# Optimization experiments

Hardware: AMD Instinct MI355X
Metric: run time of the kernel (lower is better)

The kernel has to match this reference:

```python
import jax, jax.numpy as jnp
import numpy as np

B, S, D, H = 2, 2048, 2048, 16
HD = D // H


def setup_inputs() -> dict:
    key = jax.random.key(0)
    ks = jax.random.split(key, 9)
    scale = 0.02
    return {
        "x": jax.random.normal(ks[0], (B, S, D), dtype=jnp.float32),
        "wq_w": jax.random.normal(ks[1], (D, D), dtype=jnp.float32) * scale,
        "wq_b": jnp.zeros((D,), dtype=jnp.float32),
        "wk_w": jax.random.normal(ks[2], (D, D), dtype=jnp.float32) * scale,
        "wk_b": jnp.zeros((D,), dtype=jnp.float32),
        "wv_w": jax.random.normal(ks[3], (D, D), dtype=jnp.float32) * scale,
        "wv_b": jnp.zeros((D,), dtype=jnp.float32),
        "wo_w": jax.random.normal(ks[4], (D, D), dtype=jnp.float32) * scale,
        "wo_b": jnp.zeros((D,), dtype=jnp.float32),
    }


def reference(x, wq_w, wq_b, wk_w, wk_b, wv_w, wv_b, wo_w, wo_b):
    # torch Linear: y = x @ W.T + b
    q = x @ wq_w.T + wq_b  # [B,S,D]
    k = x @ wk_w.T + wk_b
    v = x @ wv_w.T + wv_b
    # [B,S,D] -> [B,H,S,HD]
    q = q.reshape(B, S, H, HD).transpose(0, 2, 1, 3)
    k = k.reshape(B, S, H, HD).transpose(0, 2, 1, 3)
    v = v.reshape(B, S, H, HD).transpose(0, 2, 1, 3)
    # scores [B,H,S,S], scaled by sqrt(d_dim) as in the original (not head_dim)
    scores = jnp.einsum("bhid,bhjd->bhij", q, k) / np.float32(np.sqrt(D))
    # faithful reproduction of the module's triu/transpose masking:
    m = jnp.swapaxes(jnp.triu(scores), -2, -1)  # lower-tri, zeros elsewhere
    p = jax.nn.softmax(m, axis=-2)              # softmax over dim=-2, zeros included
    a = jnp.swapaxes(jnp.triu(p), -2, -1)       # [B,H,S,S]
    attn = jnp.einsum("bhij,bhjd->bhid", a, v)  # [B,H,S,HD]
    concat = attn.transpose(0, 2, 1, 3).reshape(B, S, D)
    return concat @ wo_w.T + wo_b
```

## Files before the change

kernel.cpp:

```cpp
#include <hip/hip_runtime.h>

#define BB 2
#define SS 2048
#define DD 2048
#define HH 16
#define HDIM 128
#define MTOK (BB*SS)
#define BHH (BB*HH)
#define NCHUNK 16
#define QKN (2*DD)

typedef __attribute__((ext_vector_type(8))) __bf16 bf16x8;
typedef __attribute__((ext_vector_type(4))) float f32x4;
typedef __attribute__((ext_vector_type(8))) int i32x8;
typedef __attribute__((ext_vector_type(4))) int i32x4;

__device__ __forceinline__ unsigned short f2bf(float f) {
  unsigned u = __float_as_uint(f);
  u += 0x7FFFu + ((u >> 16) & 1u);
  return (unsigned short)(u >> 16);
}
__device__ __forceinline__ float bf2f(unsigned short s) {
  return __uint_as_float(((unsigned)s) << 16);
}
__device__ __forceinline__ unsigned char f2e4m3(float f) {
  int pk = __builtin_amdgcn_cvt_pk_fp8_f32(f, f, 0, false);
  return (unsigned char)(pk & 0xFF);
}

#define GLOAD_LDS16(src, dst)                                                   \
  __builtin_amdgcn_global_load_lds(                                             \
      (const void __attribute__((address_space(1)))*)(src),                     \
      (void __attribute__((address_space(3)))*)(dst), 16, 0, 0)

__device__ __forceinline__ void barrier_raw() {
  asm volatile("" ::: "memory");
  __builtin_amdgcn_s_barrier();
  asm volatile("" ::: "memory");
}

__global__ void cvt_x_dual(const float* __restrict__ in,
                           unsigned short* __restrict__ outb,
                           unsigned int* __restrict__ out8, int n4) {
  int i = blockIdx.x * blockDim.x + threadIdx.x;
  if (i < n4) {
    float4 v = ((const float4*)in)[i];
    ushort4 o;
    o.x = f2bf(v.x); o.y = f2bf(v.y); o.z = f2bf(v.z); o.w = f2bf(v.w);
    ((ushort4*)outb)[i] = o;
    int p0 = __builtin_amdgcn_cvt_pk_fp8_f32(v.x, v.y, 0, false);
    int p1 = __builtin_amdgcn_cvt_pk_fp8_f32(v.z, v.w, 0, false);
    out8[i] = (unsigned)(p0 & 0xFFFF) | ((unsigned)(p1 & 0xFFFF) << 16);
  }
}

__global__ void cvt_w_all(const float* __restrict__ wq, const float* __restrict__ wk,
                          const float* __restrict__ wv, const float* __restrict__ wo,
                          const float* __restrict__ wqb, const float* __restrict__ wkb,
                          unsigned int* __restrict__ out8,
                          unsigned short* __restrict__ outb,
                          float* __restrict__ biasqk) {
  int blk = blockIdx.x;
  int tid = threadIdx.x;
  if (blk < 8192) {
    int i = blk * 256 + tid;
    int sel = i >> 20, r = i & 0xFFFFF;
    const float* src = sel == 0 ? wq : wk;
    float4 v = ((const float4*)src)[r];
    int p0 = __builtin_amdgcn_cvt_pk_fp8_f32(v.x, v.y, 0, false);
    int p1 = __builtin_amdgcn_cvt_pk_fp8_f32(v.z, v.w, 0, false);
    out8[i] = (unsigned)(p0 & 0xFFFF) | ((unsigned)(p1 & 0xFFFF) << 16);
  } else if (blk < 16384) {
    int i = (blk - 8192) * 256 + tid;
    int sel = i >> 20, r = i & 0xFFFFF;
    const float* src = sel == 0 ? wv : wo;
    float4 v = ((const float4*)src)[r];
    ushort4 o;
    o.x = f2bf(v.x); o.y = f2bf(v.y); o.z = f2bf(v.z); o.w = f2bf(v.w);
    ((ushort4*)outb)[i] = o;
  } else {
    int i = (blk - 16384) * 256 + tid;
    biasqk[i] = (i < DD) ? wqb[i] : wkb[i - DD];
  }
}

template <bool OUT_BF16>
__global__ __launch_bounds__(256, 2) void gemm_bt8(
    const __bf16* __restrict__ A, const __bf16* __restrict__ W,
    const float* __restrict__ bias, void* __restrict__ Cout,
    int M, int N, int K) {
  __shared__ unsigned char lds[2][32768];
  const int t = threadIdx.x;
  const int lane = t & 63, wave = t >> 6;
  const int quad = lane >> 4, l16 = lane & 15;
  const int m0 = blockIdx.y * 128;
  const int n0 = blockIdx.x * 128;
  const int wm = (wave & 1) * 64, wn = (wave >> 1) * 64;

  const __bf16* sA[4];
  const __bf16* sB[4];
#pragma unroll
  for (int c = 0; c < 4; ++c) {
    int L = c * 256 + t;
    int row = L >> 3, p = L & 7;
    int sc = (p ^ (row & 7)) * 8;
    sA[c] = A + (size_t)(m0 + row) * K + sc;
    sB[c] = W + (size_t)(n0 + row) * K + sc;
  }
  const int phk0 = (quad ^ (l16 & 7)) * 16;
  const int phk1 = ((4 + quad) ^ (l16 & 7)) * 16;

  f32x4 acc[4][4] = {};

  const int NT = K >> 6;

#pragma unroll
  for (int c = 0; c < 4; ++c)
    GLOAD_LDS16(sA[c], &lds[0][(c * 256 + wave * 64) * 16]);
#pragma unroll
  for (int c = 0; c < 4; ++c)
    GLOAD_LDS16(sB[c], &lds[0][16384 + (c * 256 + wave * 64) * 16]);

  for (int tt = 0; tt < NT; ++tt) {
    const int cur = tt & 1;
    const bool pf = (tt + 1 < NT);
    const int k1 = (tt + 1) << 6;

    if (pf) {
#pragma unroll
      for (int c = 0; c < 4; ++c)
        GLOAD_LDS16(sA[c] + k1, &lds[cur ^ 1][(c * 256 + wave * 64) * 16]);
      asm volatile("s_waitcnt vmcnt(4)" ::: "memory");
    } else {
      asm volatile("s_waitcnt vmcnt(0)" ::: "memory");
    }
    barrier_raw();
    {
      bf16x8 af[4], bfv[4];
#pragma unroll
      for (int mt = 0; mt < 4; ++mt)
        af[mt] = *(const bf16x8*)&lds[cur][(wm + mt * 16 + l16) * 128 + phk0];
#pragma unroll
      for (int nt = 0; nt < 4; ++nt)
        bfv[nt] =
            *(const bf16x8*)&lds[cur][16384 + (wn + nt * 16 + l16) * 128 + phk0];
      __builtin_amdgcn_s_setprio(1);
#pragma unroll
      for (int mt = 0; mt < 4; ++mt)
#pragma unroll
        for (int nt = 0; nt < 4; ++nt)
          acc[mt][nt] = __builtin_amdgcn_mfma_f32_16x16x32_bf16(
              af[mt], bfv[nt], acc[mt][nt], 0, 0, 0);
      __builtin_amdgcn_s_setprio(0);
    }

    if (pf) {
#pragma unroll
      for (int c = 0; c < 4; ++c)
        GLOAD_LDS16(sB[c] + k1, &lds[cur ^ 1][16384 + (c * 256 + wave * 64) * 16]);
    }
    barrier_raw();
    {
      bf16x8 af[4], bfv[4];
#pragma unroll
      for (int mt = 0; mt < 4; ++mt)
        af[mt] = *(const bf16x8*)&lds[cur][(wm + mt * 16 + l16) * 128 + phk1];
#pragma unroll
      for (int nt = 0; nt < 4; ++nt)
        bfv[nt] =
            *(const bf16x8*)&lds[cur][16384 + (wn + nt * 16 + l16) * 128 + phk1];
      __builtin_amdgcn_s_setprio(1);
#pragma unroll
      for (int mt = 0; mt < 4; ++mt)
#pragma unroll
        for (int nt = 0; nt < 4; ++nt)
          acc[mt][nt] = __builtin_amdgcn_mfma_f32_16x16x32_bf16(
              af[mt], bfv[nt], acc[mt][nt], 0, 0, 0);
      __builtin_amdgcn_s_setprio(0);
    }
    barrier_raw();
  }

#pragma unroll
  for (int mt = 0; mt < 4; ++mt) {
#pragma unroll
    for (int nt = 0; nt < 4; ++nt) {
      int col = n0 + wn + nt * 16 + l16;
      float bv = bias[col];
#pragma unroll
      for (int r = 0; r < 4; ++r) {
        int row = m0 + wm + mt * 16 + quad * 4 + r;
        float v = acc[mt][nt][r] + bv;
        if constexpr (OUT_BF16)
          ((unsigned short*)Cout)[(size_t)row * N + col] = f2bf(v);
        else
          ((float*)Cout)[(size_t)row * N + col] = v;
      }
    }
  }
}

__global__ __launch_bounds__(256, 2) void gemm_qk8(
    const unsigned char* __restrict__ A8, const unsigned char* __restrict__ W8,
    const float* __restrict__ bias, unsigned char* __restrict__ Cout,
    int M, int N, int K) {
  __shared__ unsigned char lds[2][32768];
  const int t = threadIdx.x;
  const int lane = t & 63, wave = t >> 6;
  const int quad = lane >> 4, l16 = lane & 15;
  const int m0 = blockIdx.y * 128;
  const int n0 = blockIdx.x * 128;
  const int wm = (wave & 1) * 64, wn = (wave >> 1) * 64;

  const unsigned char* sA[4];
  const unsigned char* sB[4];
#pragma unroll
  for (int c = 0; c < 4; ++c) {
    int L = c * 256 + t;
    int row = L >> 3, p = L & 7;
    int sc = (p ^ (row & 7)) * 16;
    sA[c] = A8 + (size_t)(m0 + row) * K + sc;
    sB[c] = W8 + (size_t)(n0 + row) * K + sc;
  }
  const int p0 = (2 * quad) ^ (l16 & 7);

  f32x4 acc[4][4] = {};

  const int NT = K >> 7;

#pragma unroll
  for (int c = 0; c < 4; ++c)
    GLOAD_LDS16(sA[c], &lds[0][(c * 256 + wave * 64) * 16]);
#pragma unroll
  for (int c = 0; c < 4; ++c)
    GLOAD_LDS16(sB[c], &lds[0][16384 + (c * 256 + wave * 64) * 16]);

  for (int tt = 0; tt < NT; ++tt) {
    const int cur = tt & 1;
    const bool pf = (tt + 1 < NT);
    const int k1 = (tt + 1) << 7;

    if (pf) {
#pragma unroll
      for (int c = 0; c < 4; ++c)
        GLOAD_LDS16(sA[c] + k1, &lds[cur ^ 1][(c * 256 + wave * 64) * 16]);
      asm volatile("s_waitcnt vmcnt(4)" ::: "memory");
    } else {
      asm volatile("s_waitcnt vmcnt(0)" ::: "memory");
    }
    barrier_raw();
    i32x8 af[4];
    {
#pragma unroll
      for (int mt = 0; mt < 4; ++mt) {
        int ra = (wm + mt * 16 + l16) * 128 + p0 * 16;
        ((i32x4*)&af[mt])[0] = *(const i32x4*)&lds[cur][ra];
        ((i32x4*)&af[mt])[1] = *(const i32x4*)&lds[cur][ra ^ 16];
      }
      i32x8 bv[2];
#pragma unroll
      for (int nt = 0; nt < 2; ++nt) {
        int rb = 16384 + (wn + nt * 16 + l16) * 128 + p0 * 16;
        ((i32x4*)&bv[nt])[0] = *(const i32x4*)&lds[cur][rb];
        ((i32x4*)&bv[nt])[1] = *(const i32x4*)&lds[cur][rb ^ 16];
      }
      __builtin_amdgcn_s_setprio(1);
#pragma unroll
      for (int mt = 0; mt < 4; ++mt)
#pragma unroll
        for (int nt = 0; nt < 2; ++nt)
          acc[mt][nt] = __builtin_amdgcn_mfma_scale_f32_16x16x128_f8f6f4(
              af[mt], bv[nt], acc[mt][nt], 0, 0, 0, 127, 0, 127);
      __builtin_amdgcn_s_setprio(0);
    }

    if (pf) {
#pragma unroll
      for (int c = 0; c < 4; ++c)
        GLOAD_LDS16(sB[c] + k1, &lds[cur ^ 1][16384 + (c * 256 + wave * 64) * 16]);
    }
    barrier_raw();
    {
      i32x8 bv[2];
#pragma unroll
      for (int nt = 0; nt < 2; ++nt) {
        int rb = 16384 + (wn + (nt + 2) * 16 + l16) * 128 + p0 * 16;
        ((i32x4*)&bv[nt])[0] = *(const i32x4*)&lds[cur][rb];
        ((i32x4*)&bv[nt])[1] = *(const i32x4*)&lds[cur][rb ^ 16];
      }
      __builtin_amdgcn_s_setprio(1);
#pragma unroll
      for (int mt = 0; mt < 4; ++mt)
#pragma unroll
        for (int nt = 0; nt < 2; ++nt)
          acc[mt][nt + 2] = __builtin_amdgcn_mfma_scale_f32_16x16x128_f8f6f4(
              af[mt], bv[nt], acc[mt][nt + 2], 0, 0, 0, 127, 0, 127);
      __builtin_amdgcn_s_setprio(0);
    }
    barrier_raw();
  }

#pragma unroll
  for (int mt = 0; mt < 4; ++mt) {
#pragma unroll
    for (int nt = 0; nt < 4; ++nt) {
      int col = n0 + wn + nt * 16 + l16;
      float bv = bias[col];
#pragma unroll
      for (int r = 0; r < 4; ++r) {
        int row = m0 + wm + mt * 16 + quad * 4 + r;
        Cout[(size_t)row * N + col] = f2e4m3(acc[mt][nt][r] + bv);
      }
    }
  }
}

__global__ __launch_bounds__(256, 4) void qk_rowsum8(
    const unsigned char* __restrict__ q8, const unsigned char* __restrict__ k8,
    float* __restrict__ denomA, float* __restrict__ denomB,
    float* __restrict__ diag) {
  __shared__ unsigned char lK[2][128 * 128];
  __shared__ float redS[4][64];
  __shared__ float redD[4][64];
  const int t = threadIdx.x;
  const int lane = t & 63, wave = t >> 6;
  const int quad = lane >> 4, l16 = lane & 15;
  const int bh = blockIdx.y;
  const int b = bh >> 4, h = bh & 15;
  const int pair = blockIdx.x >> 1;
  const int half = blockIdx.x & 1;
  const float C = 0.03187935771f;
  const f32x4 fz = {0.f, 0.f, 0.f, 0.f};

  int soff[4];
#pragma unroll
  for (int c = 0; c < 4; ++c) {
    int L = c * 256 + t;
    int row = L >> 3, p = L & 7;
    soff[c] = row * QKN + ((p ^ (row & 7)) * 16);
  }
  const int p0 = (2 * quad) ^ (l16 & 7);
  int bo[2];
#pragma unroll
  for (int nt = 0; nt < 2; ++nt)
    bo[nt] = (wave * 32 + nt * 16 + l16) * 128 + p0 * 16;

  const unsigned char* kbase = k8 + (size_t)(b * SS) * QKN + h * HDIM;

  for (int sub = 0; sub < 2; ++sub) {
    const int tile = (sub == 0) ? pair : 31 - pair;
    const int i0 = tile * 64;
    const int jbase = i0 & ~127;
    const int ntile = (SS - jbase) >> 7;

    i32x8 af[4];
    {
      const unsigned char* qbase =
          q8 + (size_t)(b * SS + i0 + l16) * QKN + h * HDIM + quad * 32;
#pragma unroll
      for (int mt = 0; mt < 4; ++mt)
        af[mt] = *(const i32x8*)(qbase + (size_t)(mt * 16) * QKN);
    }

    float rowacc[4][4] = {};

    int kidx = half;
    if (kidx < ntile) {
      {
        const unsigned char* src = kbase + (size_t)(jbase + kidx * 128) * QKN;
#pragma unroll
        for (int c = 0; c < 4; ++c)
          GLOAD_LDS16(src + soff[c], &lK[0][(c * 256 + wave * 64) * 16]);
      }
      asm volatile("s_waitcnt vmcnt(0)" ::: "memory");
      __syncthreads();
      int cur = 0;
      for (; kidx < ntile; kidx += 2, cur ^= 1) {
        if (kidx + 2 < ntile) {
          const unsigned char* src =
              kbase + (size_t)(jbase + (kidx + 2) * 128) * QKN;
#pragma unroll
          for (int c = 0; c < 4; ++c)
            GLOAD_LDS16(src + soff[c], &lK[cur ^ 1][(c * 256 + wave * 64) * 16]);
        }
        const unsigned char* lkc = lK[cur];
        const int j0 = jbase + kidx * 128;
        if (kidx == 0) {
          float dloc[4][4] = {};
#pragma unroll
          for (int nt = 0; nt < 2; ++nt) {
            i32x8 bf;
            ((i32x4*)&bf)[0] = *(const i32x4*)(lkc + bo[nt]);
            ((i32x4*)&bf)[1] = *(const i32x4*)(lkc + (bo[nt] ^ 16));
            f32x4 acc[4];
#pragma unroll
            for (int mt = 0; mt < 4; ++mt)
              acc[mt] = __builtin_amdgcn_mfma_scale_f32_16x16x128_f8f6f4(
                  af[mt], bf, fz, 0, 0, 0, 127, 0, 127);
            const int colg = j0 + wave * 32 + nt * 16 + l16;
#pragma unroll
            for (int mt = 0; mt < 4; ++mt)
#pragma unroll
              for (int r = 0; r < 4; ++r) {
                int rg = i0 + mt * 16 + quad * 4 + r;
                float e = (colg >= rg)
                              ? __builtin_amdgcn_exp2f(acc[mt][r] * C) : 0.f;
                rowacc[mt][r] += e;
                if (colg == rg) dloc[mt][r] = e;
              }
          }
#pragma unroll
          for (int mt = 0; mt < 4; ++mt)
#pragma unroll
            for (int r = 0; r < 4; ++r) {
              float d = dloc[mt][r];
#pragma unroll
              for (int off = 1; off < 16; off <<= 1) d += __shfl_xor(d, off, 64);
              if (l16 == 0) redD[wave][mt * 16 + quad * 4 + r] = d;
            }
        } else {
#pragma unroll
          for (int nt = 0; nt < 2; ++nt) {
            i32x8 bf;
            ((i32x4*)&bf)[0] = *(const i32x4*)(lkc + bo[nt]);
            ((i32x4*)&bf)[1] = *(const i32x4*)(lkc + (bo[nt] ^ 16));
            f32x4 acc[4];
#pragma unroll
            for (int mt = 0; mt < 4; ++mt)
              acc[mt] = __builtin_amdgcn_mfma_scale_f32_16x16x128_f8f6f4(
                  af[mt], bf, fz, 0, 0, 0, 127, 0, 127);
#pragma unroll
            for (int mt = 0; mt < 4; ++mt)
#pragma unroll
              for (int r = 0; r < 4; ++r)
                rowacc[mt][r] += __builtin_amdgcn_exp2f(acc[mt][r] * C);
          }
        }
        asm volatile("s_waitcnt vmcnt(0)" ::: "memory");
        __syncthreads();
      }
    }

    __syncthreads();
#pragma unroll
    for (int mt = 0; mt < 4; ++mt)
#pragma unroll
      for (int r = 0; r < 4; ++r) {
        float s = rowacc[mt][r];
#pragma unroll
        for (int off = 1; off < 16; off <<= 1) s += __shfl_xor(s, off, 64);
        if (l16 == 0) redS[wave][mt * 16 + quad * 4 + r] = s;
      }
    __syncthreads();
    if (t < 64) {
      const int rg = i0 + t;
      float s = redS[0][t] + redS[1][t] + redS[2][t] + redS[3][t];
      if (half == 0) {
        denomA[bh * SS + rg] = (float)rg + s;
        diag[bh * SS + rg] = redD[0][t] + redD[1][t] + redD[2][t] + redD[3][t];
      } else {
        denomB[bh * SS + rg] = s;
      }
    }
  }
}

__global__ void scan_pass1(const __bf16* __restrict__ v0,
                           float* __restrict__ csum) {
  int blk = blockIdx.x;
  int bh = blk >> 4, c = blk & 15;
  int b = bh >> 4, h = bh & 15;
  int t = threadIdx.x;
  int rs = t >> 4, dg = t & 15;
  const unsigned short* base = (const unsigned short*)v0 +
      (size_t)(b * SS + c * 128 + rs * 8) * DD + h * HDIM + dg * 8;
  float s[8] = {0.f, 0.f, 0.f, 0.f, 0.f, 0.f, 0.f, 0.f};
#pragma unroll
  for (int i = 0; i < 8; ++i) {
    uint4 u = *(const uint4*)(base + (size_t)i * DD);
    const unsigned short* us = (const unsigned short*)&u;
#pragma unroll
    for (int j = 0; j < 8; ++j) s[j] += bf2f(us[j]);
  }
  __shared__ float red[16 * 128];
#pragma unroll
  for (int j = 0; j < 8; ++j) red[rs * 128 + dg * 8 + j] = s[j];
  __syncthreads();
  for (int st = 8; st >= 1; st >>= 1) {
    if (rs < st) {
#pragma unroll
      for (int j = 0; j < 8; ++j)
        red[rs * 128 + dg * 8 + j] += red[(rs + st) * 128 + dg * 8 + j];
    }
    __syncthreads();
  }
  if (rs == 0) {
#pragma unroll
    for (int j = 0; j < 8; ++j)
      csum[(size_t)blk * 128 + dg * 8 + j] = red[dg * 8 + j];
  }
}

__global__ void scan_pass2(const __bf16* __restrict__ v0,
                           const float* __restrict__ csum,
                           const float* __restrict__ denomA,
                           const float* __restrict__ denomB,
                           const float* __restrict__ diag,
                           unsigned short* __restrict__ ctx) {
  int blk = blockIdx.x;
  int bh = blk >> 4, c = blk & 15;
  int b = bh >> 4, h = bh & 15;
  int t = threadIdx.x;
  int rs = t >> 4, dg = t & 15;
  const unsigned short* vbase = (const unsigned short*)v0 +
      (size_t)(b * SS + c * 128 + rs * 8) * DD + h * HDIM + dg * 8;
  float vrow[8][8];
  float ls[8] = {0.f, 0.f, 0.f, 0.f, 0.f, 0.f, 0.f, 0.f};
#pragma unroll
  for (int i = 0; i < 8; ++i) {
    uint4 u = *(const uint4*)(vbase + (size_t)i * DD);
    const unsigned short* us = (const unsigned short*)&u;
#pragma unroll
    for (int j = 0; j < 8; ++j) {
      vrow[i][j] = bf2f(us[j]);
      ls[j] += vrow[i][j];
    }
  }
  __shared__ float red[16 * 128];
#pragma unroll
  for (int j = 0; j < 8; ++j) red[rs * 128 + dg * 8 + j] = ls[j];
  __syncthreads();

  float pre[8] = {0.f, 0.f, 0.f, 0.f, 0.f, 0.f, 0.f, 0.f};
  for (int cc = 0; cc < c; ++cc) {
    const float* cp = csum + (size_t)(bh * 16 + cc) * 128 + dg * 8;
#pragma unroll
    for (int j = 0; j < 8; ++j) pre[j] += cp[j];
  }
  for (int ss2 = 0; ss2 < rs; ++ss2) {
#pragma unroll
    for (int j = 0; j < 8; ++j) pre[j] += red[ss2 * 128 + dg * 8 + j];
  }

  int row0 = c * 128 + rs * 8;
  unsigned short* obase =
      ctx + (size_t)(b * SS + row0) * DD + h * HDIM + dg * 8;
  const float* dnA = denomA + bh * SS + row0;
  const float* dnB = denomB + bh * SS + row0;
  const float* dgp = diag + bh * SS + row0;
#pragma unroll
  for (int i = 0; i < 8; ++i) {
    float inv = 1.0f / (dnA[i] + dnB[i]);
    float dv = dgp[i];
    unsigned short o[8];
#pragma unroll
    for (int j = 0; j < 8; ++j) {
      float val = (pre[j] + dv * vrow[i][j]) * inv;
      o[j] = f2bf(val);
      pre[j] += vrow[i][j];
    }
    *(uint4*)(obase + (size_t)i * DD) = *(const uint4*)o;
  }
}

extern "C" void kernel_launch(void* const* d_in, const int* in_sizes, int n_in,
                              void* d_out, int out_size, void* d_ws, size_t ws_size,
                              hipStream_t stream) {
  (void)in_sizes; (void)n_in; (void)out_size; (void)ws_size;
  const float* x    = (const float*)d_in[0];
  const float* wq_w = (const float*)d_in[1];
  const float* wq_b = (const float*)d_in[2];
  const float* wk_w = (const float*)d_in[3];
  const float* wk_b = (const float*)d_in[4];
  const float* wv_w = (const float*)d_in[5];
  const float* wv_b = (const float*)d_in[6];
  const float* wo_w = (const float*)d_in[7];
  const float* wo_b = (const float*)d_in[8];

  char* ws = (char*)d_ws;
  size_t off = 0;
  auto alloc = [&](size_t bytes) {
    char* p = ws + off;
    off += (bytes + 255) & ~(size_t)255;
    return p;
  };
  unsigned short* xb   = (unsigned short*)alloc((size_t)MTOK * DD * 2);
  unsigned char*  x8   = (unsigned char*)alloc((size_t)MTOK * DD);
  unsigned char*  wqk8 = (unsigned char*)alloc((size_t)2 * DD * DD);
  unsigned short* wvo  = (unsigned short*)alloc((size_t)2 * DD * DD * 2);
  unsigned char*  qk8  = (unsigned char*)alloc((size_t)MTOK * QKN);
  unsigned short* v    = (unsigned short*)alloc((size_t)MTOK * DD * 2);
  unsigned short* ctx  = (unsigned short*)alloc((size_t)MTOK * DD * 2);
  float* biasqk = (float*)alloc((size_t)2 * DD * 4);
  float* denomA = (float*)alloc((size_t)BHH * SS * 4);
  float* denomB = (float*)alloc((size_t)BHH * SS * 4);
  float* diag   = (float*)alloc((size_t)BHH * SS * 4);
  float* csum   = (float*)alloc((size_t)BHH * NCHUNK * 128 * 4);

  {
    int n4 = MTOK * DD / 4;
    cvt_x_dual<<<n4 / 256, 256, 0, stream>>>(x, xb, (unsigned int*)x8, n4);
    cvt_w_all<<<16400, 256, 0, stream>>>(wq_w, wk_w, wv_w, wo_w, wq_b, wk_b,
                                         (unsigned int*)wqk8, wvo, biasqk);
  }

  gemm_qk8<<<dim3(QKN / 128, MTOK / 128), 256, 0, stream>>>(
      x8, wqk8, biasqk, qk8, MTOK, QKN, DD);

  gemm_bt8<true><<<dim3(DD / 128, MTOK / 128), 256, 0, stream>>>(
      (const __bf16*)xb, (const __bf16*)wvo, wv_b, v, MTOK, DD, DD);

  qk_rowsum8<<<dim3(32, BHH), 256, 0, stream>>>(
      qk8,
      qk8 + DD,
      denomA, denomB, diag);

  scan_pass1<<<BHH * NCHUNK, 256, 0, stream>>>((const __bf16*)v, csum);
  scan_pass2<<<BHH * NCHUNK, 256, 0, stream>>>((const __bf16*)v, csum,
                                               denomA, denomB, diag, ctx);

  gemm_bt8<false><<<dim3(DD / 128, MTOK / 128), 256, 0, stream>>>(
      (const __bf16*)ctx, (const __bf16*)(wvo + (size_t)DD * DD), wo_b,
      d_out, MTOK, DD, DD);
}
```

Measured before the change: 310.7 us.

## Load GEMM A operand directly to registers, stage only weights in LDS

Both the bf16 and fp8 GEMM kernels stop staging the A tile through shared memory. Each wave now reads its A fragments straight from global memory into registers, and only the weight tile is double-buffered in LDS. This halves LDS per block, which allows launch bounds of 4 blocks per CU, and it merges the two half-step barriers per K tile into one. The cost is that A rows are reread from global/L2 by each of the two wave columns instead of being shared. The A loads are also issued right before use with no prefetch, so their latency may be exposed.

Result: slower. 546.3 us (+75.9%).

```diff
diff --git a/kernel.cpp b/kernel.cpp
--- a/kernel.cpp
+++ b/kernel.cpp
@@ -85,11 +85,11 @@
 }
 
 template <bool OUT_BF16>
-__global__ __launch_bounds__(256, 2) void gemm_bt8(
+__global__ __launch_bounds__(256, 4) void gemm_bt8(
     const __bf16* __restrict__ A, const __bf16* __restrict__ W,
     const float* __restrict__ bias, void* __restrict__ Cout,
     int M, int N, int K) {
-  __shared__ unsigned char lds[2][32768];
+  __shared__ unsigned char lds[2][16384];
   const int t = threadIdx.x;
   const int lane = t & 63, wave = t >> 6;
   const int quad = lane >> 4, l16 = lane & 15;
@@ -97,16 +97,14 @@
   const int n0 = blockIdx.x * 128;
   const int wm = (wave & 1) * 64, wn = (wave >> 1) * 64;
 
-  const __bf16* sA[4];
   const __bf16* sB[4];
 #pragma unroll
   for (int c = 0; c < 4; ++c) {
     int L = c * 256 + t;
     int row = L >> 3, p = L & 7;
-    int sc = (p ^ (row & 7)) * 8;
-    sA[c] = A + (size_t)(m0 + row) * K + sc;
-    sB[c] = W + (size_t)(n0 + row) * K + sc;
-  }
+    sB[c] = W + (size_t)(n0 + row) * K + ((p ^ (row & 7)) * 8);
+  }
+  const __bf16* aptr = A + (size_t)(m0 + wm + l16) * K + quad * 8;
   const int phk0 = (quad ^ (l16 & 7)) * 16;
   const int phk1 = ((4 + quad) ^ (l16 & 7)) * 16;
 
@@ -116,66 +114,49 @@
 
 #pragma unroll
   for (int c = 0; c < 4; ++c)
-    GLOAD_LDS16(sA[c], &lds[0][(c * 256 + wave * 64) * 16]);
-#pragma unroll
-  for (int c = 0; c < 4; ++c)
-    GLOAD_LDS16(sB[c], &lds[0][16384 + (c * 256 + wave * 64) * 16]);
+    GLOAD_LDS16(sB[c], &lds[0][(c * 256 + wave * 64) * 16]);
 
   for (int tt = 0; tt < NT; ++tt) {
     const int cur = tt & 1;
     const bool pf = (tt + 1 < NT);
+    const int k0 = tt << 6;
     const int k1 = (tt + 1) << 6;
 
+    bf16x8 af[4][2];
+#pragma unroll
+    for (int mt = 0; mt < 4; ++mt) {
+      af[mt][0] = *(const bf16x8*)(aptr + (size_t)(mt * 16) * K + k0);
+      af[mt][1] = *(const bf16x8*)(aptr + (size_t)(mt * 16) * K + k0 + 32);
+    }
     if (pf) {
 #pragma unroll
       for (int c = 0; c < 4; ++c)
-        GLOAD_LDS16(sA[c] + k1, &lds[cur ^ 1][(c * 256 + wave * 64) * 16]);
+        GLOAD_LDS16(sB[c] + k1, &lds[cur ^ 1][(c * 256 + wave * 64) * 16]);
       asm volatile("s_waitcnt vmcnt(4)" ::: "memory");
     } else {
       asm volatile("s_waitcnt vmcnt(0)" ::: "memory");
     }
     barrier_raw();
     {
-      bf16x8 af[4], bfv[4];
-#pragma unroll
-      for (int mt = 0; mt < 4; ++mt)
-        af[mt] = *(const bf16x8*)&lds[cur][(wm + mt * 16 + l16) * 128 + phk0];
-#pragma unroll
-      for (int nt = 0; nt < 4; ++nt)
-        bfv[nt] =
-            *(const bf16x8*)&lds[cur][16384 + (wn + nt * 16 + l16) * 128 + phk0];
+      bf16x8 bv0[4], bv1[4];
+#pragma unroll
+      for (int nt = 0; nt < 4; ++nt) {
+        bv0[nt] = *(const bf16x8*)&lds[cur][(wn + nt * 16 + l16) * 128 + phk0];
+        bv1[nt] = *(const bf16x8*)&lds[cur][(wn + nt * 16 + l16) * 128 + phk1];
+      }
       __builtin_amdgcn_s_setprio(1);
 #pragma unroll
       for (int mt = 0; mt < 4; ++mt)
 #pragma unroll
         for (int nt = 0; nt < 4; ++nt)
           acc[mt][nt] = __builtin_amdgcn_mfma_f32_16x16x32_bf16(
-              af[mt], bfv[nt], acc[mt][nt], 0, 0, 0);
-      __builtin_amdgcn_s_setprio(0);
-    }
-
-    if (pf) {
-#pragma unroll
-      for (int c = 0; c < 4; ++c)
-        GLOAD_LDS16(sB[c] + k1, &lds[cur ^ 1][16384 + (c * 256 + wave * 64) * 16]);
-    }
-    barrier_raw();
-    {
-      bf16x8 af[4], bfv[4];
-#pragma unroll
-      for (int mt = 0; mt < 4; ++mt)
-        af[mt] = *(const bf16x8*)&lds[cur][(wm + mt * 16 + l16) * 128 + phk1];
-#pragma unroll
-      for (int nt = 0; nt < 4; ++nt)
-        bfv[nt] =
-            *(const bf16x8*)&lds[cur][16384 + (wn + nt * 16 + l16) * 128 + phk1];
-      __builtin_amdgcn_s_setprio(1);
+              af[mt][0], bv0[nt], acc[mt][nt], 0, 0, 0);
 #pragma unroll
       for (int mt = 0; mt < 4; ++mt)
 #pragma unroll
         for (int nt = 0; nt < 4; ++nt)
           acc[mt][nt] = __builtin_amdgcn_mfma_f32_16x16x32_bf16(
-              af[mt], bfv[nt], acc[mt][nt], 0, 0, 0);
+              af[mt][1], bv1[nt], acc[mt][nt], 0, 0, 0);
       __builtin_amdgcn_s_setprio(0);
     }
     barrier_raw();
@@ -200,11 +181,11 @@
   }
 }
 
-__global__ __launch_bounds__(256, 2) void gemm_qk8(
+__global__ __launch_bounds__(256, 4) void gemm_qk8(
     const unsigned char* __restrict__ A8, const unsigned char* __restrict__ W8,
     const float* __restrict__ bias, unsigned char* __restrict__ Cout,
     int M, int N, int K) {
-  __shared__ unsigned char lds[2][32768];
+  __shared__ unsigned char lds[2][16384];
   const int t = threadIdx.x;
   const int lane = t & 63, wave = t >> 6;
   const int quad = lane >> 4, l16 = lane & 15;
@@ -212,16 +193,14 @@
   const int n0 = blockIdx.x * 128;
   const int wm = (wave & 1) * 64, wn = (wave >> 1) * 64;
 
-  const unsigned char* sA[4];
   const unsigned char* sB[4];
 #pragma unroll
   for (int c = 0; c < 4; ++c) {
     int L = c * 256 + t;
     int row = L >> 3, p = L & 7;
-    int sc = (p ^ (row & 7)) * 16;
-    sA[c] = A8 + (size_t)(m0 + row) * K + sc;
-    sB[c] = W8 + (size_t)(n0 + row) * K + sc;
-  }
+    sB[c] = W8 + (size_t)(n0 + row) * K + ((p ^ (row & 7)) * 16);
+  }
+  const unsigned char* aptr = A8 + (size_t)(m0 + wm + l16) * K + quad * 32;
   const int p0 = (2 * quad) ^ (l16 & 7);
 
   f32x4 acc[4][4] = {};
@@ -230,37 +209,32 @@
 
 #pragma unroll
   for (int c = 0; c < 4; ++c)
-    GLOAD_LDS16(sA[c], &lds[0][(c * 256 + wave * 64) * 16]);
-#pragma unroll
-  for (int c = 0; c < 4; ++c)
-    GLOAD_LDS16(sB[c], &lds[0][16384 + (c * 256 + wave * 64) * 16]);
+    GLOAD_LDS16(sB[c], &lds[0][(c * 256 + wave * 64) * 16]);
 
   for (int tt = 0; tt < NT; ++tt) {
     const int cur = tt & 1;
     const bool pf = (tt + 1 < NT);
+    const int k0 = tt << 7;
     const int k1 = (tt + 1) << 7;
 
+    i32x8 af[4];
+#pragma unroll
+    for (int mt = 0; mt < 4; ++mt)
+      af[mt] = *(const i32x8*)(aptr + (size_t)(mt * 16) * K + k0);
     if (pf) {
 #pragma unroll
       for (int c = 0; c < 4; ++c)
-        GLOAD_LDS16(sA[c] + k1, &lds[cur ^ 1][(c * 256 + wave * 64) * 16]);
+        GLOAD_LDS16(sB[c] + k1, &lds[cur ^ 1][(c * 256 + wave * 64) * 16]);
       asm volatile("s_waitcnt vmcnt(4)" ::: "memory");
     } else {
       asm volatile("s_waitcnt vmcnt(0)" ::: "memory");
     }
     barrier_raw();
-    i32x8 af[4];
     {
-#pragma unroll
-      for (int mt = 0; mt < 4; ++mt) {
-        int ra = (wm + mt * 16 + l16) * 128 + p0 * 16;
-        ((i32x4*)&af[mt])[0] = *(const i32x4*)&lds[cur][ra];
-        ((i32x4*)&af[mt])[1] = *(const i32x4*)&lds[cur][ra ^ 16];
-      }
-      i32x8 bv[2];
-#pragma unroll
-      for (int nt = 0; nt < 2; ++nt) {
-        int rb = 16384 + (wn + nt * 16 + l16) * 128 + p0 * 16;
+      i32x8 bv[4];
+#pragma unroll
+      for (int nt = 0; nt < 4; ++nt) {
+        int rb = (wn + nt * 16 + l16) * 128 + p0 * 16;
         ((i32x4*)&bv[nt])[0] = *(const i32x4*)&lds[cur][rb];
         ((i32x4*)&bv[nt])[1] = *(const i32x4*)&lds[cur][rb ^ 16];
       }
@@ -268,33 +242,9 @@
 #pragma unroll
       for (int mt = 0; mt < 4; ++mt)
 #pragma unroll
-        for (int nt = 0; nt < 2; ++nt)
+        for (int nt = 0; nt < 4; ++nt)
           acc[mt][nt] = __builtin_amdgcn_mfma_scale_f32_16x16x128_f8f6f4(
               af[mt], bv[nt], acc[mt][nt], 0, 0, 0, 127, 0, 127);
-      __builtin_amdgcn_s_setprio(0);
-    }
-
-    if (pf) {
-#pragma unroll
-      for (int c = 0; c < 4; ++c)
-        GLOAD_LDS16(sB[c] + k1, &lds[cur ^ 1][16384 + (c * 256 + wave * 64) * 16]);
-    }
-    barrier_raw();
-    {
-      i32x8 bv[2];
-#pragma unroll
-      for (int nt = 0; nt < 2; ++nt) {
-        int rb = 16384 + (wn + (nt + 2) * 16 + l16) * 128 + p0 * 16;
-        ((i32x4*)&bv[nt])[0] = *(const i32x4*)&lds[cur][rb];
-        ((i32x4*)&bv[nt])[1] = *(const i32x4*)&lds[cur][rb ^ 16];
-      }
-      __builtin_amdgcn_s_setprio(1);
-#pragma unroll
-      for (int mt = 0; mt < 4; ++mt)
-#pragma unroll
-        for (int nt = 0; nt < 2; ++nt)
-          acc[mt][nt + 2] = __builtin_amdgcn_mfma_scale_f32_16x16x128_f8f6f4(
-              af[mt], bv[nt], acc[mt][nt + 2], 0, 0, 0, 127, 0, 127);
       __builtin_amdgcn_s_setprio(0);
     }
     barrier_raw();
```
